# Kernel tuning notes

Measured on AMD Instinct MI355X. Metric: run time of the kernel, lower is better.

## Reference

```python
import jax, jax.numpy as jnp
import numpy as np

N_NODES = 50000
N_EDGES = 500000
HIDDEN = 128
HEADS = 8
HEAD_DIM = HIDDEN // HEADS
EPS = 1e-16  # PyG softmax denominator epsilon


def _kaiming(key, shape):
    fan_in = shape[0]
    return jax.random.normal(key, shape, dtype=jnp.float32) * np.sqrt(2.0 / fan_in)


def prelu(x, a):
    return jnp.maximum(x, 0.0) + a * jnp.minimum(x, 0.0)


def transformer_conv(x, src, dst, Wq, bq, Wk, bk, Wv, bv, Ws, bs):
    """PyG TransformerConv (concat=True, root_weight=True, beta=False), eval mode."""
    N = x.shape[0]
    q = (x @ Wq + bq).reshape(N, HEADS, HEAD_DIM)
    k = (x @ Wk + bk).reshape(N, HEADS, HEAD_DIM)
    v = (x @ Wv + bv).reshape(N, HEADS, HEAD_DIM)
    # per-edge attention: query from destination, key/value from source
    score = jnp.einsum('ehd,ehd->eh', q[dst], k[src]) / np.sqrt(HEAD_DIM)  # [E,H]
    m = jax.ops.segment_max(score, dst, num_segments=N)                     # [N,H]
    e = jnp.exp(score - m[dst])
    s = jax.ops.segment_sum(e, dst, num_segments=N)
    alpha = e / (s[dst] + EPS)                                              # [E,H]
    agg = jax.ops.segment_sum(alpha[..., None] * v[src], dst, num_segments=N)
    return agg.reshape(N, HIDDEN) + x @ Ws + bs  # skip connection (lin_skip)


def setup_inputs() -> dict:
    key = jax.random.key(0)
    ks = jax.random.split(key, 12)
    inp = {
        'x': jax.random.normal(ks[0], (N_NODES, HIDDEN), dtype=jnp.float32),
        'edge_index': jax.random.randint(ks[1], (2, N_EDGES), 0, N_NODES, dtype=jnp.int64 if jax.config.jax_enable_x64 else jnp.int32),
        'prelu_w': jnp.full((1,), 0.25, dtype=jnp.float32),
    }
    i = 2
    for layer in (1, 2):
        for nm in ('q', 'k', 'v', 's'):
            inp[f'W{nm}{layer}'] = _kaiming(ks[i], (HIDDEN, HIDDEN))
            inp[f'b{nm}{layer}'] = jnp.zeros((HIDDEN,), dtype=jnp.float32)
            i += 1
        ks = jax.random.split(ks[-1], 12)
        i = 0
    return inp


def reference(x, edge_index, prelu_w,
              Wq1, bq1, Wk1, bk1, Wv1, bv1, Ws1, bs1,
              Wq2, bq2, Wk2, bk2, Wv2, bv2, Ws2, bs2):
    src, dst = edge_index[0], edge_index[1]
    o = transformer_conv(x, src, dst, Wq1, bq1, Wk1, bk1, Wv1, bv1, Ws1, bs1)
    o = prelu(o, prelu_w)
    o = transformer_conv(o, src, dst, Wq2, bq2, Wk2, bk2, Wv2, bv2, Ws2, bs2)
    o = o + x  # residual
    return prelu(o, prelu_w)
```

## Files before the change

### kernel.cpp

```cpp
#include <hip/hip_runtime.h>

#define NN 50000
#define NE 500000
#define HID 128
#define MT 782

typedef __attribute__((ext_vector_type(8))) short short8;
typedef __attribute__((ext_vector_type(4))) float f32x4;
typedef unsigned short ushort_t;
typedef unsigned int uint32;

__device__ __forceinline__ float bflo(uint32 u) {
    union { float f; uint32 i; } x; x.i = u << 16; return x.f;
}
__device__ __forceinline__ float bfhi(uint32 u) {
    union { float f; uint32 i; } x; x.i = u & 0xffff0000u; return x.f;
}
__device__ __forceinline__ ushort_t f2bf(float f) {
    union { float f; uint32 i; } x; x.f = f;
    uint32 r = x.i + 0x7FFFu + ((x.i >> 16) & 1u);
    return (ushort_t)(r >> 16);
}

__global__ void pack_w2(const float* __restrict__ Wq1, const float* __restrict__ Wk1,
                        const float* __restrict__ Wv1, const float* __restrict__ Ws1,
                        const float* __restrict__ Wq2, const float* __restrict__ Wk2,
                        const float* __restrict__ Wv2, const float* __restrict__ Ws2,
                        ushort_t* __restrict__ Bt1, ushort_t* __restrict__ Bt2)
{
    int idx = blockIdx.x * 256 + threadIdx.x;
    int layer = idx >> 16;
    int r = idx & 65535;
    int col = r >> 7;
    int kk = r & 127;
    int wsel = col >> 7;
    const float* W = (layer == 0)
        ? ((wsel == 0) ? Wq1 : (wsel == 1) ? Wk1 : (wsel == 2) ? Wv1 : Ws1)
        : ((wsel == 0) ? Wq2 : (wsel == 1) ? Wk2 : (wsel == 2) ? Wv2 : Ws2);
    (layer == 0 ? Bt1 : Bt2)[r] = f2bf(W[kk * HID + (col & 127)]);
}

template <int LAYER>
__global__ __launch_bounds__(256, 5) void gemm_mfma(
    const float* __restrict__ Xf, const ushort_t* __restrict__ Xh,
    const ushort_t* __restrict__ Bt,
    const float* __restrict__ bqp, const float* __restrict__ bkp,
    const float* __restrict__ bvp, const float* __restrict__ bsp,
    ushort_t* __restrict__ Qb, ushort_t* __restrict__ KVb, ushort_t* __restrict__ Sfb)
{
    __shared__ ushort_t As[64 * 128];
    __shared__ ushort_t Bs[64 * 128];
    const int wgid = blockIdx.x;
    const int xcd = wgid & 7, kidx = wgid >> 3;
    const int local = xcd * MT + kidx;
    const int mtile = local >> 3;
    const int gg = local & 7;
    const int g = gg >> 1;
    const int colbase = (gg & 1) * 64;
    const int Mbase = mtile * 64;
    const int tid = threadIdx.x;
    const int lane = tid & 63, wave = tid >> 6;

    #pragma unroll
    for (int it = 0; it < 4; ++it) {
        int lin = it * 256 + tid;
        int row = lin >> 4, s = lin & 15;
        int rg = Mbase + row; if (rg >= NN) rg = NN - 1;
        short8 v;
        if (LAYER == 1) {
            float4 f0 = *reinterpret_cast<const float4*>(Xf + (size_t)rg * HID + s * 8);
            float4 f1 = *reinterpret_cast<const float4*>(Xf + (size_t)rg * HID + s * 8 + 4);
            v[0] = (short)f2bf(f0.x); v[1] = (short)f2bf(f0.y);
            v[2] = (short)f2bf(f0.z); v[3] = (short)f2bf(f0.w);
            v[4] = (short)f2bf(f1.x); v[5] = (short)f2bf(f1.y);
            v[6] = (short)f2bf(f1.z); v[7] = (short)f2bf(f1.w);
        } else {
            v = *reinterpret_cast<const short8*>(Xh + (size_t)rg * HID + s * 8);
        }
        *reinterpret_cast<short8*>((char*)As + row * 256 + ((s * 16) ^ ((row & 7) * 16))) = v;
    }
    #pragma unroll
    for (int it = 0; it < 4; ++it) {
        int lin = it * 256 + tid;
        int col = lin >> 4, s = lin & 15;
        short8 v = *reinterpret_cast<const short8*>(
            Bt + (size_t)(g * 128 + colbase + col) * HID + s * 8);
        *reinterpret_cast<short8*>((char*)Bs + col * 256 + ((s * 16) ^ ((col & 7) * 16))) = v;
    }
    __syncthreads();

    const int l15 = lane & 15;
    const int wrow = wave * 16;
    f32x4 acc[4] = {};
    #pragma unroll
    for (int kk = 0; kk < 4; ++kk) {
        int kbyte = kk * 64 + (lane >> 4) * 16;
        int ar = wrow + l15;
        short8 a = *reinterpret_cast<const short8*>(
            (const char*)As + ar * 256 + (kbyte ^ ((ar & 7) * 16)));
        #pragma unroll
        for (int nb = 0; nb < 4; ++nb) {
            int c = nb * 16 + l15;
            short8 b = *reinterpret_cast<const short8*>(
                (const char*)Bs + c * 256 + (kbyte ^ ((c & 7) * 16)));
            acc[nb] = __builtin_amdgcn_mfma_f32_16x16x32_bf16(a, b, acc[nb], 0, 0, 0);
        }
    }
    __syncthreads();

    const float* bias = (g == 0) ? bqp : (g == 1) ? bkp : (g == 2) ? bvp : bsp;
    float* Cs = reinterpret_cast<float*>(As);
    #pragma unroll
    for (int nb = 0; nb < 4; ++nb) {
        int c = nb * 16 + l15;
        float bb = bias[colbase + c];
        #pragma unroll
        for (int r = 0; r < 4; ++r) {
            int rl = wrow + (lane >> 4) * 4 + r;
            Cs[rl * 64 + c] = acc[nb][r] + bb;
        }
    }
    __syncthreads();

    #pragma unroll
    for (int it = 0; it < 2; ++it) {
        int lin = it * 256 + tid;
        int row = lin >> 3, s = lin & 7;
        int rg = Mbase + row;
        if (rg < NN) {
            float4 v0 = *reinterpret_cast<float4*>(&Cs[row * 64 + s * 8]);
            float4 v1 = *reinterpret_cast<float4*>(&Cs[row * 64 + s * 8 + 4]);
            short8 o;
            o[0] = (short)f2bf(v0.x); o[1] = (short)f2bf(v0.y);
            o[2] = (short)f2bf(v0.z); o[3] = (short)f2bf(v0.w);
            o[4] = (short)f2bf(v1.x); o[5] = (short)f2bf(v1.y);
            o[6] = (short)f2bf(v1.z); o[7] = (short)f2bf(v1.w);
            ushort_t* dst = (g == 0) ? (Qb  + (size_t)rg * HID + colbase + s * 8)
                          : (g == 1) ? (KVb + (size_t)rg * 256 + colbase + s * 8)
                          : (g == 2) ? (KVb + (size_t)rg * 256 + 128 + colbase + s * 8)
                          :            (Sfb + (size_t)rg * HID + colbase + s * 8);
            *reinterpret_cast<short8*>(dst) = o;
        }
    }
}

__global__ void zero_i32(int* __restrict__ p, int n)
{
    int i = blockIdx.x * blockDim.x + threadIdx.x;
    if (i < n) p[i] = 0;
}

__global__ void hist_kernel(const int* __restrict__ dst, int* __restrict__ counts)
{
    int e = blockIdx.x * blockDim.x + threadIdx.x;
    if (e < NE) atomicAdd(&counts[dst[e]], 1);
}

#define SCAN_B 196

__global__ __launch_bounds__(256) void block_sums(const int* __restrict__ counts,
                                                  int* __restrict__ bsum)
{
    int i = blockIdx.x * 256 + threadIdx.x;
    int v = (i < NN) ? counts[i] : 0;
    #pragma unroll
    for (int o = 1; o < 64; o <<= 1) v += __shfl_xor(v, o);
    __shared__ int ws[4];
    if ((threadIdx.x & 63) == 0) ws[threadIdx.x >> 6] = v;
    __syncthreads();
    if (threadIdx.x == 0) bsum[blockIdx.x] = ws[0] + ws[1] + ws[2] + ws[3];
}

__global__ __launch_bounds__(256) void scan_bsums(const int* __restrict__ bsum,
                                                  int* __restrict__ bbase)
{
    __shared__ int sh[256];
    int t = threadIdx.x;
    int v = (t < SCAN_B) ? bsum[t] : 0;
    sh[t] = v;
    __syncthreads();
    for (int o = 1; o < 256; o <<= 1) {
        int u = (t >= o) ? sh[t - o] : 0;
        __syncthreads();
        sh[t] += u;
        __syncthreads();
    }
    bbase[t] = (t > 0) ? sh[t - 1] : 0;
}

__global__ __launch_bounds__(256) void write_offsets(const int* __restrict__ counts,
        const int* __restrict__ bbase, int* __restrict__ offsets, int* __restrict__ cursor)
{
    __shared__ int sh[256];
    int t = threadIdx.x;
    int i = blockIdx.x * 256 + t;
    int v = (i < NN) ? counts[i] : 0;
    sh[t] = v;
    __syncthreads();
    for (int o = 1; o < 256; o <<= 1) {
        int u = (t >= o) ? sh[t - o] : 0;
        __syncthreads();
        sh[t] += u;
        __syncthreads();
    }
    int excl = sh[t] - v + bbase[blockIdx.x];
    if (i < NN) { offsets[i] = excl; cursor[i] = excl; }
    if (i == NN - 1) offsets[NN] = excl + v;
}

__global__ void scatter_kernel(const int* __restrict__ src, const int* __restrict__ dst,
                               int* __restrict__ cursor, int* __restrict__ csr_src)
{
    int e = blockIdx.x * blockDim.x + threadIdx.x;
    if (e < NE) {
        int pos = atomicAdd(&cursor[dst[e]], 1);
        csr_src[pos] = src[e];
    }
}

template <int LAYER>
__global__ __launch_bounds__(256) void edge_aggregate(
    const ushort_t* __restrict__ Qb, const ushort_t* __restrict__ KVb,
    const ushort_t* __restrict__ Sfb,
    const int* __restrict__ offsets, const int* __restrict__ csr_src,
    const float* __restrict__ xres, const float* __restrict__ prelu_w,
    float* __restrict__ outF, ushort_t* __restrict__ outB)
{
    const int lane = threadIdx.x & 63;
    const int wid  = __builtin_amdgcn_readfirstlane((int)(threadIdx.x >> 6));
    const int node = blockIdx.x * 4 + wid;
    const int d2 = lane * 2;

    uint32 qu = *reinterpret_cast<const uint32*>(Qb + (size_t)node * HID + d2);
    const float q0 = bflo(qu) * 0.25f;
    const float q1 = bfhi(qu) * 0.25f;

    const int beg = offsets[node];
    const int end = offsets[node + 1];

    float den = 0.f, a0 = 0.f, a1 = 0.f;

#define COMPUTE(KU, VU) {                                                      \
        float p = q0 * bflo(KU) + q1 * bfhi(KU);                               \
        p += __shfl_xor(p, 1); p += __shfl_xor(p, 2); p += __shfl_xor(p, 4);   \
        float w = __expf(p);                                                   \
        den += w;                                                              \
        a0 += w * bflo(VU);                                                    \
        a1 += w * bfhi(VU); }

    int i = beg;
    for (; i + 8 <= end; i += 8) {
        uint32 ku[8], vu[8];
        #pragma unroll
        for (int j = 0; j < 8; ++j) {
            int s = csr_src[i + j];
            const ushort_t* kv = KVb + (size_t)s * 256;
            ku[j] = *reinterpret_cast<const uint32*>(kv + d2);
            vu[j] = *reinterpret_cast<const uint32*>(kv + 128 + d2);
        }
        #pragma unroll
        for (int j = 0; j < 8; ++j) COMPUTE(ku[j], vu[j])
    }
    for (; i + 4 <= end; i += 4) {
        uint32 ku[4], vu[4];
        #pragma unroll
        for (int j = 0; j < 4; ++j) {
            int s = csr_src[i + j];
            const ushort_t* kv = KVb + (size_t)s * 256;
            ku[j] = *reinterpret_cast<const uint32*>(kv + d2);
            vu[j] = *reinterpret_cast<const uint32*>(kv + 128 + d2);
        }
        #pragma unroll
        for (int j = 0; j < 4; ++j) COMPUTE(ku[j], vu[j])
    }
    for (; i < end; ++i) {
        int s = csr_src[i];
        const ushort_t* kv = KVb + (size_t)s * 256;
        uint32 ku = *reinterpret_cast<const uint32*>(kv + d2);
        uint32 vu = *reinterpret_cast<const uint32*>(kv + 128 + d2);
        COMPUTE(ku, vu)
    }
#undef COMPUTE

    float inv = (den > 0.f) ? 1.f / den : 0.f;
    uint32 su = *reinterpret_cast<const uint32*>(Sfb + (size_t)node * HID + d2);
    float r0 = a0 * inv + bflo(su);
    float r1 = a1 * inv + bfhi(su);
    if (LAYER == 2) {
        float2 xr = *reinterpret_cast<const float2*>(xres + (size_t)node * HID + d2);
        r0 += xr.x; r1 += xr.y;
    }
    const float al = prelu_w[0];
    r0 = fmaxf(r0, 0.f) + al * fminf(r0, 0.f);
    r1 = fmaxf(r1, 0.f) + al * fminf(r1, 0.f);
    if (LAYER == 1) {
        uint32 o = (uint32)f2bf(r0) | ((uint32)f2bf(r1) << 16);
        *reinterpret_cast<uint32*>(outB + (size_t)node * HID + d2) = o;
    } else {
        float2 o; o.x = r0; o.y = r1;
        *reinterpret_cast<float2*>(outF + (size_t)node * HID + d2) = o;
    }
}

extern "C" void kernel_launch(void* const* d_in, const int* in_sizes, int n_in,
                              void* d_out, int out_size, void* d_ws, size_t ws_size,
                              hipStream_t stream)
{
    const float* x       = (const float*)d_in[0];
    const int*   ei      = (const int*)d_in[1];
    const float* prelu_w = (const float*)d_in[2];
    const float* Wq1 = (const float*)d_in[3],  *bq1 = (const float*)d_in[4];
    const float* Wk1 = (const float*)d_in[5],  *bk1 = (const float*)d_in[6];
    const float* Wv1 = (const float*)d_in[7],  *bv1 = (const float*)d_in[8];
    const float* Ws1 = (const float*)d_in[9],  *bs1 = (const float*)d_in[10];
    const float* Wq2 = (const float*)d_in[11], *bq2 = (const float*)d_in[12];
    const float* Wk2 = (const float*)d_in[13], *bk2 = (const float*)d_in[14];
    const float* Wv2 = (const float*)d_in[15], *bv2 = (const float*)d_in[16];
    const float* Ws2 = (const float*)d_in[17], *bs2 = (const float*)d_in[18];

    char* w = (char*)d_ws;
    size_t off = 0;
    auto alloc = [&](size_t bytes) { void* p = w + off; off += (bytes + 255) & ~(size_t)255; return p; };
    ushort_t* x1b  = (ushort_t*)alloc((size_t)NN * HID * 2);
    ushort_t* Qb   = (ushort_t*)alloc((size_t)NN * HID * 2);
    ushort_t* KVb  = (ushort_t*)alloc((size_t)NN * 256 * 2);
    ushort_t* Sfb  = (ushort_t*)alloc((size_t)NN * HID * 2);
    ushort_t* Bt1  = (ushort_t*)alloc((size_t)512 * 128 * 2);
    ushort_t* Bt2  = (ushort_t*)alloc((size_t)512 * 128 * 2);
    int* counts  = (int*)alloc(NN * sizeof(int));
    int* bsum    = (int*)alloc(256 * sizeof(int));
    int* bbase   = (int*)alloc(256 * sizeof(int));
    int* offsets = (int*)alloc((NN + 1) * sizeof(int));
    int* cursor  = (int*)alloc(NN * sizeof(int));
    int* csr_src = (int*)alloc(NE * sizeof(int));
    (void)ws_size; (void)in_sizes; (void)n_in; (void)out_size;

    const int* srcIdx = ei;
    const int* dstIdx = ei + NE;

    zero_i32<<<(NN + 255) / 256, 256, 0, stream>>>(counts, NN);
    hist_kernel<<<(NE + 255) / 256, 256, 0, stream>>>(dstIdx, counts);
    block_sums<<<SCAN_B, 256, 0, stream>>>(counts, bsum);
    scan_bsums<<<1, 256, 0, stream>>>(bsum, bbase);
    write_offsets<<<SCAN_B, 256, 0, stream>>>(counts, bbase, offsets, cursor);
    scatter_kernel<<<(NE + 255) / 256, 256, 0, stream>>>(srcIdx, dstIdx, cursor, csr_src);

    pack_w2<<<512, 256, 0, stream>>>(Wq1, Wk1, Wv1, Ws1, Wq2, Wk2, Wv2, Ws2, Bt1, Bt2);

    const int ggemm = 8 * MT;

    gemm_mfma<1><<<ggemm, 256, 0, stream>>>(x, nullptr, Bt1, bq1, bk1, bv1, bs1,
                                            Qb, KVb, Sfb);
    edge_aggregate<1><<<NN / 4, 256, 0, stream>>>(Qb, KVb, Sfb, offsets, csr_src,
                                                  nullptr, prelu_w, nullptr, x1b);
    gemm_mfma<2><<<ggemm, 256, 0, stream>>>(nullptr, x1b, Bt2, bq2, bk2, bv2, bs2,
                                            Qb, KVb, Sfb);
    edge_aggregate<2><<<NN / 4, 256, 0, stream>>>(Qb, KVb, Sfb, offsets, csr_src,
                                                  x, prelu_w, (float*)d_out, nullptr);
}
```

Measured before the change: 194.2 us.

## Switch to fp16 storage and process two edges per wave in aggregation

Replaces bf16 with fp16 for the packed weights, the projected Q/K/V/skip tensors and the layer-1 activations. The GEMM now uses the fp16 MFMA, and the 1/sqrt(head_dim) scale is folded into the Q weights and bias. The edge aggregation kernel is restructured so each half-wave handles a different edge with 4 channels per lane, and the halves are combined by cross-lane shuffles at the end. This aims to raise memory-level parallelism and cut instruction count per edge in the gather loop. The cost is possible fp16 overflow or precision risk and an extra reduction step.

```diff
diff --git a/kernel.cpp b/kernel.cpp
--- a/kernel.cpp
+++ b/kernel.cpp
@@ -6,20 +6,18 @@
 #define MT 782
 
 typedef __attribute__((ext_vector_type(8))) short short8;
+typedef __attribute__((ext_vector_type(8))) _Float16 half8;
+typedef __attribute__((ext_vector_type(2))) _Float16 half2v;
 typedef __attribute__((ext_vector_type(4))) float f32x4;
 typedef unsigned short ushort_t;
 typedef unsigned int uint32;
-
-__device__ __forceinline__ float bflo(uint32 u) {
-    union { float f; uint32 i; } x; x.i = u << 16; return x.f;
-}
-__device__ __forceinline__ float bfhi(uint32 u) {
-    union { float f; uint32 i; } x; x.i = u & 0xffff0000u; return x.f;
-}
-__device__ __forceinline__ ushort_t f2bf(float f) {
-    union { float f; uint32 i; } x; x.f = f;
-    uint32 r = x.i + 0x7FFFu + ((x.i >> 16) & 1u);
-    return (ushort_t)(r >> 16);
+typedef _Float16 half_t;
+
+__device__ __forceinline__ ushort_t f2h(float f) {
+    union { half_t h; ushort_t u; } x; x.h = (half_t)f; return x.u;
+}
+__device__ __forceinline__ half2v u2h2(uint32 u) {
+    union { uint32 u; half2v h; } x; x.u = u; return x.h;
 }
 
 __global__ void pack_w2(const float* __restrict__ Wq1, const float* __restrict__ Wk1,
@@ -37,7 +35,9 @@
     const float* W = (layer == 0)
         ? ((wsel == 0) ? Wq1 : (wsel == 1) ? Wk1 : (wsel == 2) ? Wv1 : Ws1)
         : ((wsel == 0) ? Wq2 : (wsel == 1) ? Wk2 : (wsel == 2) ? Wv2 : Ws2);
-    (layer == 0 ? Bt1 : Bt2)[r] = f2bf(W[kk * HID + (col & 127)]);
+    float val = W[kk * HID + (col & 127)];
+    if (wsel == 0) val *= 0.25f;
+    (layer == 0 ? Bt1 : Bt2)[r] = f2h(val);
 }
 
 template <int LAYER>
@@ -70,10 +70,10 @@
         if (LAYER == 1) {
             float4 f0 = *reinterpret_cast<const float4*>(Xf + (size_t)rg * HID + s * 8);
             float4 f1 = *reinterpret_cast<const float4*>(Xf + (size_t)rg * HID + s * 8 + 4);
-            v[0] = (short)f2bf(f0.x); v[1] = (short)f2bf(f0.y);
-            v[2] = (short)f2bf(f0.z); v[3] = (short)f2bf(f0.w);
-            v[4] = (short)f2bf(f1.x); v[5] = (short)f2bf(f1.y);
-            v[6] = (short)f2bf(f1.z); v[7] = (short)f2bf(f1.w);
+            v[0] = (short)f2h(f0.x); v[1] = (short)f2h(f0.y);
+            v[2] = (short)f2h(f0.z); v[3] = (short)f2h(f0.w);
+            v[4] = (short)f2h(f1.x); v[5] = (short)f2h(f1.y);
+            v[6] = (short)f2h(f1.z); v[7] = (short)f2h(f1.w);
         } else {
             v = *reinterpret_cast<const short8*>(Xh + (size_t)rg * HID + s * 8);
         }
@@ -96,14 +96,14 @@
     for (int kk = 0; kk < 4; ++kk) {
         int kbyte = kk * 64 + (lane >> 4) * 16;
         int ar = wrow + l15;
-        short8 a = *reinterpret_cast<const short8*>(
+        half8 a = *reinterpret_cast<const half8*>(
             (const char*)As + ar * 256 + (kbyte ^ ((ar & 7) * 16)));
         #pragma unroll
         for (int nb = 0; nb < 4; ++nb) {
             int c = nb * 16 + l15;
-            short8 b = *reinterpret_cast<const short8*>(
+            half8 b = *reinterpret_cast<const half8*>(
                 (const char*)Bs + c * 256 + (kbyte ^ ((c & 7) * 16)));
-            acc[nb] = __builtin_amdgcn_mfma_f32_16x16x32_bf16(a, b, acc[nb], 0, 0, 0);
+            acc[nb] = __builtin_amdgcn_mfma_f32_16x16x32_f16(a, b, acc[nb], 0, 0, 0);
         }
     }
     __syncthreads();
@@ -114,6 +114,7 @@
     for (int nb = 0; nb < 4; ++nb) {
         int c = nb * 16 + l15;
         float bb = bias[colbase + c];
+        if (g == 0) bb *= 0.25f;
         #pragma unroll
         for (int r = 0; r < 4; ++r) {
             int rl = wrow + (lane >> 4) * 4 + r;
@@ -131,10 +132,10 @@
             float4 v0 = *reinterpret_cast<float4*>(&Cs[row * 64 + s * 8]);
             float4 v1 = *reinterpret_cast<float4*>(&Cs[row * 64 + s * 8 + 4]);
             short8 o;
-            o[0] = (short)f2bf(v0.x); o[1] = (short)f2bf(v0.y);
-            o[2] = (short)f2bf(v0.z); o[3] = (short)f2bf(v0.w);
-            o[4] = (short)f2bf(v1.x); o[5] = (short)f2bf(v1.y);
-            o[6] = (short)f2bf(v1.z); o[7] = (short)f2bf(v1.w);
+            o[0] = (short)f2h(v0.x); o[1] = (short)f2h(v0.y);
+            o[2] = (short)f2h(v0.z); o[3] = (short)f2h(v0.w);
+            o[4] = (short)f2h(v1.x); o[5] = (short)f2h(v1.y);
+            o[6] = (short)f2h(v1.z); o[7] = (short)f2h(v1.w);
             ushort_t* dst = (g == 0) ? (Qb  + (size_t)rg * HID + colbase + s * 8)
                           : (g == 1) ? (KVb + (size_t)rg * 256 + colbase + s * 8)
                           : (g == 2) ? (KVb + (size_t)rg * 256 + 128 + colbase + s * 8)
@@ -220,85 +221,106 @@
 
 template <int LAYER>
 __global__ __launch_bounds__(256) void edge_aggregate(
-    const ushort_t* __restrict__ Qb, const ushort_t* __restrict__ KVb,
-    const ushort_t* __restrict__ Sfb,
+    const half_t* __restrict__ Qh, const half_t* __restrict__ KVh,
+    const half_t* __restrict__ Sh,
     const int* __restrict__ offsets, const int* __restrict__ csr_src,
     const float* __restrict__ xres, const float* __restrict__ prelu_w,
-    float* __restrict__ outF, ushort_t* __restrict__ outB)
+    float* __restrict__ outF, ushort_t* __restrict__ outH)
 {
     const int lane = threadIdx.x & 63;
     const int wid  = __builtin_amdgcn_readfirstlane((int)(threadIdx.x >> 6));
     const int node = blockIdx.x * 4 + wid;
-    const int d2 = lane * 2;
-
-    uint32 qu = *reinterpret_cast<const uint32*>(Qb + (size_t)node * HID + d2);
-    const float q0 = bflo(qu) * 0.25f;
-    const float q1 = bfhi(qu) * 0.25f;
+    const bool hi  = lane >= 32;
+    const int  c   = lane & 31;
+
+    uint2 qu = *reinterpret_cast<const uint2*>(Qh + (size_t)node * HID + c * 4);
+    half2v qa = u2h2(qu.x), qb = u2h2(qu.y);
+    const float q0 = (float)qa[0], q1 = (float)qa[1];
+    const float q2 = (float)qb[0], q3 = (float)qb[1];
 
     const int beg = offsets[node];
     const int end = offsets[node + 1];
 
-    float den = 0.f, a0 = 0.f, a1 = 0.f;
+    float den = 0.f, a0 = 0.f, a1 = 0.f, a2 = 0.f, a3 = 0.f;
 
 #define COMPUTE(KU, VU) {                                                      \
-        float p = q0 * bflo(KU) + q1 * bfhi(KU);                               \
-        p += __shfl_xor(p, 1); p += __shfl_xor(p, 2); p += __shfl_xor(p, 4);   \
+        half2v k01 = u2h2((KU).x), k23 = u2h2((KU).y);                         \
+        float p = (float)k01[0] * q0 + (float)k01[1] * q1                      \
+                + (float)k23[0] * q2 + (float)k23[1] * q3;                     \
+        p += __shfl_xor(p, 1); p += __shfl_xor(p, 2);                          \
         float w = __expf(p);                                                   \
         den += w;                                                              \
-        a0 += w * bflo(VU);                                                    \
-        a1 += w * bfhi(VU); }
+        half2v v01 = u2h2((VU).x), v23 = u2h2((VU).y);                         \
+        a0 += w * (float)v01[0]; a1 += w * (float)v01[1];                      \
+        a2 += w * (float)v23[0]; a3 += w * (float)v23[1]; }
 
     int i = beg;
     for (; i + 8 <= end; i += 8) {
-        uint32 ku[8], vu[8];
-        #pragma unroll
-        for (int j = 0; j < 8; ++j) {
-            int s = csr_src[i + j];
-            const ushort_t* kv = KVb + (size_t)s * 256;
-            ku[j] = *reinterpret_cast<const uint32*>(kv + d2);
-            vu[j] = *reinterpret_cast<const uint32*>(kv + 128 + d2);
-        }
-        #pragma unroll
-        for (int j = 0; j < 8; ++j) COMPUTE(ku[j], vu[j])
-    }
-    for (; i + 4 <= end; i += 4) {
-        uint32 ku[4], vu[4];
+        uint2 ku[4], vu[4];
         #pragma unroll
         for (int j = 0; j < 4; ++j) {
-            int s = csr_src[i + j];
-            const ushort_t* kv = KVb + (size_t)s * 256;
-            ku[j] = *reinterpret_cast<const uint32*>(kv + d2);
-            vu[j] = *reinterpret_cast<const uint32*>(kv + 128 + d2);
+            int s = hi ? csr_src[i + 2 * j + 1] : csr_src[i + 2 * j];
+            const half_t* kv = KVh + (size_t)s * 256 + c * 4;
+            ku[j] = *reinterpret_cast<const uint2*>(kv);
+            vu[j] = *reinterpret_cast<const uint2*>(kv + 128);
         }
         #pragma unroll
         for (int j = 0; j < 4; ++j) COMPUTE(ku[j], vu[j])
     }
-    for (; i < end; ++i) {
+    for (; i + 2 <= end; i += 2) {
+        int s = hi ? csr_src[i + 1] : csr_src[i];
+        const half_t* kv = KVh + (size_t)s * 256 + c * 4;
+        uint2 ku = *reinterpret_cast<const uint2*>(kv);
+        uint2 vu = *reinterpret_cast<const uint2*>(kv + 128);
+        COMPUTE(ku, vu)
+    }
+    if (i < end) {
         int s = csr_src[i];
-        const ushort_t* kv = KVb + (size_t)s * 256;
-        uint32 ku = *reinterpret_cast<const uint32*>(kv + d2);
-        uint32 vu = *reinterpret_cast<const uint32*>(kv + 128 + d2);
-        COMPUTE(ku, vu)
+        const half_t* kv = KVh + (size_t)s * 256 + c * 4;
+        uint2 ku = *reinterpret_cast<const uint2*>(kv);
+        uint2 vu = *reinterpret_cast<const uint2*>(kv + 128);
+        half2v k01 = u2h2(ku.x), k23 = u2h2(ku.y);
+        float p = (float)k01[0] * q0 + (float)k01[1] * q1
+                + (float)k23[0] * q2 + (float)k23[1] * q3;
+        p += __shfl_xor(p, 1); p += __shfl_xor(p, 2);
+        float w = hi ? 0.f : __expf(p);
+        den += w;
+        half2v v01 = u2h2(vu.x), v23 = u2h2(vu.y);
+        a0 += w * (float)v01[0]; a1 += w * (float)v01[1];
+        a2 += w * (float)v23[0]; a3 += w * (float)v23[1];
     }
 #undef COMPUTE
 
-    float inv = (den > 0.f) ? 1.f / den : 0.f;
-    uint32 su = *reinterpret_cast<const uint32*>(Sfb + (size_t)node * HID + d2);
-    float r0 = a0 * inv + bflo(su);
-    float r1 = a1 * inv + bfhi(su);
-    if (LAYER == 2) {
-        float2 xr = *reinterpret_cast<const float2*>(xres + (size_t)node * HID + d2);
-        r0 += xr.x; r1 += xr.y;
-    }
-    const float al = prelu_w[0];
-    r0 = fmaxf(r0, 0.f) + al * fminf(r0, 0.f);
-    r1 = fmaxf(r1, 0.f) + al * fminf(r1, 0.f);
-    if (LAYER == 1) {
-        uint32 o = (uint32)f2bf(r0) | ((uint32)f2bf(r1) << 16);
-        *reinterpret_cast<uint32*>(outB + (size_t)node * HID + d2) = o;
-    } else {
-        float2 o; o.x = r0; o.y = r1;
-        *reinterpret_cast<float2*>(outF + (size_t)node * HID + d2) = o;
+    den += __shfl_xor(den, 32);
+    a0 += __shfl_xor(a0, 32); a1 += __shfl_xor(a1, 32);
+    a2 += __shfl_xor(a2, 32); a3 += __shfl_xor(a3, 32);
+
+    if (!hi) {
+        float inv = (den > 0.f) ? 1.f / den : 0.f;
+        uint2 su = *reinterpret_cast<const uint2*>(Sh + (size_t)node * HID + c * 4);
+        half2v s01 = u2h2(su.x), s23 = u2h2(su.y);
+        float r0 = a0 * inv + (float)s01[0];
+        float r1 = a1 * inv + (float)s01[1];
+        float r2 = a2 * inv + (float)s23[0];
+        float r3 = a3 * inv + (float)s23[1];
+        if (LAYER == 2) {
+            float4 xr = *reinterpret_cast<const float4*>(xres + (size_t)node * HID + c * 4);
+            r0 += xr.x; r1 += xr.y; r2 += xr.z; r3 += xr.w;
+        }
+        const float al = prelu_w[0];
+        r0 = fmaxf(r0, 0.f) + al * fminf(r0, 0.f);
+        r1 = fmaxf(r1, 0.f) + al * fminf(r1, 0.f);
+        r2 = fmaxf(r2, 0.f) + al * fminf(r2, 0.f);
+        r3 = fmaxf(r3, 0.f) + al * fminf(r3, 0.f);
+        if (LAYER == 1) {
+            uint2 o;
+            o.x = (uint32)f2h(r0) | ((uint32)f2h(r1) << 16);
+            o.y = (uint32)f2h(r2) | ((uint32)f2h(r3) << 16);
+            *reinterpret_cast<uint2*>(outH + (size_t)node * HID + c * 4) = o;
+        } else {
+            float4 o; o.x = r0; o.y = r1; o.z = r2; o.w = r3;
+            *reinterpret_cast<float4*>(outF + (size_t)node * HID + c * 4) = o;
+        }
     }
 }
 
@@ -321,7 +343,7 @@
     char* w = (char*)d_ws;
     size_t off = 0;
     auto alloc = [&](size_t bytes) { void* p = w + off; off += (bytes + 255) & ~(size_t)255; return p; };
-    ushort_t* x1b  = (ushort_t*)alloc((size_t)NN * HID * 2);
+    ushort_t* x1h  = (ushort_t*)alloc((size_t)NN * HID * 2);
     ushort_t* Qb   = (ushort_t*)alloc((size_t)NN * HID * 2);
     ushort_t* KVb  = (ushort_t*)alloc((size_t)NN * 256 * 2);
     ushort_t* Sfb  = (ushort_t*)alloc((size_t)NN * HID * 2);
@@ -351,10 +373,12 @@
 
     gemm_mfma<1><<<ggemm, 256, 0, stream>>>(x, nullptr, Bt1, bq1, bk1, bv1, bs1,
                                             Qb, KVb, Sfb);
-    edge_aggregate<1><<<NN / 4, 256, 0, stream>>>(Qb, KVb, Sfb, offsets, csr_src,
-                                                  nullptr, prelu_w, nullptr, x1b);
-    gemm_mfma<2><<<ggemm, 256, 0, stream>>>(nullptr, x1b, Bt2, bq2, bk2, bv2, bs2,
+    edge_aggregate<1><<<NN / 4, 256, 0, stream>>>((const half_t*)Qb, (const half_t*)KVb,
+                                                  (const half_t*)Sfb, offsets, csr_src,
+                                                  nullptr, prelu_w, nullptr, x1h);
+    gemm_mfma<2><<<ggemm, 256, 0, stream>>>(nullptr, x1h, Bt2, bq2, bk2, bv2, bs2,
                                             Qb, KVb, Sfb);
-    edge_aggregate<2><<<NN / 4, 256, 0, stream>>>(Qb, KVb, Sfb, offsets, csr_src,
+    edge_aggregate<2><<<NN / 4, 256, 0, stream>>>((const half_t*)Qb, (const half_t*)KVb,
+                                                  (const half_t*)Sfb, offsets, csr_src,
                                                   x, prelu_w, (float*)d_out, nullptr);
 }
```

Result: slower. 204.9 us (+5.5%).
